# Optimization experiments

Hardware: AMD Instinct MI355X
Metric: run time of the kernel (lower is better)

The kernel has to match this reference:

```python
import jax, jax.numpy as jnp
import numpy as np

B, L, E = 4, 2048, 1024
H, HS = 16, 64  # head_num, head_size; E == H*HS


def setup_inputs() -> dict:
    key = jax.random.key(0)
    k1, k2, k3 = jax.random.split(key, 3)
    x = jax.random.normal(k1, (B, L, E), dtype=jnp.float32)
    W_attn = jax.random.normal(k2, (E, 3 * H * HS), dtype=jnp.float32) * (E ** -0.5)
    W_ffn = jax.random.normal(k3, (H * HS, E), dtype=jnp.float32) * ((H * HS) ** -0.5)
    return {"x": x, "W_attn": W_attn, "W_ffn": W_ffn}


def reference(x, W_attn, W_ffn):
    b, l, _ = x.shape
    z = x @ W_attn  # [B, L, 3*H*HS]
    # NOTE: original splits as (k, q, v) in that order
    k, q, v = jnp.split(z, 3, axis=2)
    k = k.reshape(b, l, H, HS).transpose(0, 2, 1, 3)  # [B,H,L,HS]
    q = q.reshape(b, l, H, HS).transpose(0, 2, 1, 3)
    v = v.reshape(b, l, H, HS).transpose(0, 2, 1, 3)
    # scores[i, j] = k_i . q_j (k plays the row role, q the column role)
    scores = jnp.einsum('bhid,bhjd->bhij', k, q) / (HS ** 0.5)
    idx = jnp.arange(l)
    causal = idx[None, :] > idx[:, None]  # True where j > i (masked out)
    scores = jnp.where(causal[None, None], -jnp.inf, scores)
    attn = jax.nn.softmax(scores, axis=-1)  # softmax over j (the q index)
    y = jnp.einsum('bhij,bhjd->bhid', attn, v)  # [B,H,L,HS]
    y = y.transpose(0, 2, 1, 3).reshape(b, l, H * HS)
    return y @ W_ffn
```

## Files before the change

### kernel.cpp

```cpp
#include <hip/hip_runtime.h>
#include <hip/hip_bf16.h>

typedef __attribute__((ext_vector_type(8))) short bf16x8;
typedef __attribute__((ext_vector_type(4))) float f32x4;

__device__ __forceinline__ short f2b(float f) {
    unsigned u = __builtin_bit_cast(unsigned, f);
    unsigned r = (u + 0x7FFFu + ((u >> 16) & 1u)) >> 16;
    return (short)r;
}

__device__ __forceinline__ unsigned cvt_pk_bf16(float lo, float hi) {
    unsigned r;
    asm("v_cvt_pk_bf16_f32 %0, %1, %2" : "=v"(r) : "v"(lo), "v"(hi));
    return r;
}

__device__ __forceinline__ void gload_lds16(const void* g, void* l) {
    __builtin_amdgcn_global_load_lds((const __attribute__((address_space(1))) unsigned*)g,
                                     (__attribute__((address_space(3))) unsigned*)l, 16, 0, 0);
}

__global__ void conv_swz(const float* __restrict__ in, short* __restrict__ out, long nch) {
    long i = (long)blockIdx.x * blockDim.x + threadIdx.x;
    long stride = (long)gridDim.x * blockDim.x;
    for (; i < nch; i += stride) {
        long m = i >> 7;
        int ch = (int)(i & 127);
        int p = (ch & ~7) | ((ch ^ (int)m) & 7);
        const float4* s = (const float4*)(in + i * 8);
        float4 a = s[0], b = s[1];
        bf16x8 ov;
        ov[0] = f2b(a.x); ov[1] = f2b(a.y); ov[2] = f2b(a.z); ov[3] = f2b(a.w);
        ov[4] = f2b(b.x); ov[5] = f2b(b.y); ov[6] = f2b(b.z); ov[7] = f2b(b.w);
        *(bf16x8*)(out + (m << 10) + p * 8) = ov;
    }
}

__global__ void transpose_swz(const float* __restrict__ in, short* __restrict__ outT, int R, int C) {
    __shared__ float t[32][33];
    int c0 = blockIdx.x * 32, r0 = blockIdx.y * 32;
    int tx = threadIdx.x, ty = threadIdx.y;
    #pragma unroll
    for (int j = 0; j < 4; ++j)
        t[ty + j * 8][tx] = in[(long)(r0 + ty + j * 8) * C + c0 + tx];
    __syncthreads();
    #pragma unroll
    for (int j = 0; j < 4; ++j) {
        int n = c0 + ty + j * 8;
        int k = r0 + tx;
        int kp = (k & ~63) | ((((k >> 3) ^ n) & 7) << 3) | (k & 7);
        outT[(long)n * R + kp] = f2b(t[tx][ty + j * 8]);
    }
}

template<int MODE>
__launch_bounds__(256, 2)
__global__ void gemm_nt(const short* __restrict__ A, const short* __restrict__ Bt,
                        int M, int N, int K,
                        short* __restrict__ qrole, short* __restrict__ krole,
                        short* __restrict__ vT, float* __restrict__ out) {
    __shared__ __align__(16) short As[128][64];
    __shared__ __align__(16) short Bs[128][64];
    const int tid = threadIdx.x;
    const int lane = tid & 63;
    const int wid = tid >> 6;
    const int wm = wid >> 1, wn = wid & 1;
    const int m0 = blockIdx.y * 128, n0 = blockIdx.x * 128;
    const int r16 = lane & 15, g = lane >> 4;
    const int sw = r16 & 7;
    const char* Ab = (const char*)A;
    const char* Bb = (const char*)Bt;
    const long Kb = (long)K * 2;
    f32x4 acc[4][4] = {};
    for (int k0 = 0; k0 < K; k0 += 64) {
        #pragma unroll
        for (int it = 0; it < 4; ++it) {
            int id = it * 256 + tid;
            int r = id >> 3, cch = id & 7;
            gload_lds16(Ab + (long)(m0 + r) * Kb + k0 * 2 + cch * 16, (char*)As + id * 16);
            gload_lds16(Bb + (long)(n0 + r) * Kb + k0 * 2 + cch * 16, (char*)Bs + id * 16);
        }
        __syncthreads();
        #pragma unroll
        for (int kk = 0; kk < 2; ++kk) {
            bf16x8 af[4], bfr[4];
            #pragma unroll
            for (int m = 0; m < 4; ++m)
                af[m] = *(const bf16x8*)&As[wm * 64 + m * 16 + r16][((kk * 4 + g) ^ sw) * 8];
            #pragma unroll
            for (int n = 0; n < 4; ++n)
                bfr[n] = *(const bf16x8*)&Bs[wn * 64 + n * 16 + r16][((kk * 4 + g) ^ sw) * 8];
            #pragma unroll
            for (int m = 0; m < 4; ++m)
                #pragma unroll
                for (int n = 0; n < 4; ++n)
                    acc[m][n] = __builtin_amdgcn_mfma_f32_16x16x32_bf16(af[m], bfr[n], acc[m][n], 0, 0, 0);
        }
        __syncthreads();
    }
    #pragma unroll
    for (int m = 0; m < 4; ++m) {
        #pragma unroll
        for (int n = 0; n < 4; ++n) {
            #pragma unroll
            for (int r = 0; r < 4; ++r) {
                int row = m0 + wm * 64 + m * 16 + g * 4 + r;
                int col = n0 + wn * 64 + n * 16 + r16;
                float v = acc[m][n][r];
                if (MODE == 0) {
                    int which = col >> 10, cc = col & 1023;
                    int h = cc >> 6, d = cc & 63;
                    int b = row >> 11, li = row & 2047;
                    int bh = b * 16 + h;
                    if (which == 0)      qrole[((long)bh * 2048 + li) * 64 + d] = f2b(v * 0.18033688f);
                    else if (which == 1) krole[((long)bh * 2048 + li) * 64 + (d ^ ((li & 7) << 3))] = f2b(v);
                    else                 vT[((long)bh * 64 + d) * 2048 + ((li & ~63) | ((li & 63) ^ ((d & 7) << 3)))] = f2b(v);
                } else {
                    out[(long)row * N + col] = v;
                }
            }
        }
    }
}

__launch_bounds__(256, 3)
__global__ void attn_kernel(const short* __restrict__ qrole, const short* __restrict__ krole,
                            const short* __restrict__ vT, short* __restrict__ y) {
    __shared__ __align__(16) short K_lds[2][64][64];
    __shared__ __align__(16) short V_lds[2][64][64];
    __shared__ __align__(16) short P_lds[4][16][72];
    const int tid = threadIdx.x, lane = tid & 63, w = tid >> 6;
    const int r16 = lane & 15, g = lane >> 4;
    const int idb = blockIdx.x;
    const int bh = idb & 63;
    const int c = 15 - (idb >> 6);
    const int q0 = c << 7;
    const int T = 2 * c + 2;
    const short* qb = qrole + (long)bh * (2048 * 64);
    const char* kbyte = (const char*)(krole + (long)bh * (2048 * 64));
    const char* vbyte = (const char*)(vT + (long)bh * (64 * 2048));
    const int b = bh >> 4, h = bh & 15;

    bf16x8 qf[2][2];
    #pragma unroll
    for (int m = 0; m < 2; ++m)
        #pragma unroll
        for (int ks = 0; ks < 2; ++ks)
            qf[m][ks] = *(const bf16x8*)&qb[(long)(q0 + m * 64 + w * 16 + r16) * 64 + ks * 32 + g * 8];

    f32x4 o[2][4] = {};
    float mr[2], lr[2];
    #pragma unroll
    for (int m = 0; m < 2; ++m) { mr[m] = -1e30f; lr[m] = 0.f; }

    {
        char* kdst = (char*)&K_lds[0][0][0];
        char* vdst = (char*)&V_lds[0][0][0];
        #pragma unroll
        for (int it = 0; it < 2; ++it) {
            int cid = it * 256 + tid;
            long r = cid >> 3; int cch = cid & 7;
            gload_lds16(kbyte + r * 128 + cch * 16, kdst + cid * 16);
            gload_lds16(vbyte + r * 4096 + cch * 16, vdst + cid * 16);
        }
    }

    for (int t = 0; t < T; ++t) {
        __syncthreads();
        const int cur = t & 1;
        if (t + 1 < T) {
            const long jn = (long)(t + 1) << 6;
            char* kdst = (char*)&K_lds[cur ^ 1][0][0];
            char* vdst = (char*)&V_lds[cur ^ 1][0][0];
            #pragma unroll
            for (int it = 0; it < 2; ++it) {
                int cid = it * 256 + tid;
                long r = cid >> 3; int cch = cid & 7;
                gload_lds16(kbyte + (jn + r) * 128 + cch * 16, kdst + cid * 16);
                gload_lds16(vbyte + r * 4096 + jn * 2 + cch * 16, vdst + cid * 16);
            }
        }
        const int jt = t << 6;
        const char* kbase = (const char*)&K_lds[cur][0][0];
        const char* vbase = (const char*)&V_lds[cur][0][0];
        const int swz = (r16 & 7) << 4;

        #pragma unroll
        for (int m = 0; m < 2; ++m) {
            const int qbase = q0 + m * 64 + w * 16;
            if (jt > qbase + 15) continue;

            f32x4 s[4] = {};
            #pragma unroll
            for (int ks = 0; ks < 2; ++ks)
                #pragma unroll
                for (int n = 0; n < 4; ++n) {
                    bf16x8 kf = *(const bf16x8*)(kbase + (n * 16 + r16) * 128 + ((ks * 64 + g * 16) ^ swz));
                    s[n] = __builtin_amdgcn_mfma_f32_16x16x32_bf16(kf, qf[m][ks], s[n], 0, 0, 0);
                }
            if (jt + 63 > qbase) {
                const int i = qbase + r16;
                #pragma unroll
                for (int n = 0; n < 4; ++n)
                    #pragma unroll
                    for (int r = 0; r < 4; ++r)
                        if (jt + n * 16 + g * 4 + r > i) s[n][r] = -1e30f;
            }
            float tm = s[0][0];
            #pragma unroll
            for (int n = 0; n < 4; ++n)
                #pragma unroll
                for (int r = 0; r < 4; ++r)
                    tm = fmaxf(tm, s[n][r]);
            tm = fmaxf(tm, __shfl_xor(tm, 16));
            tm = fmaxf(tm, __shfl_xor(tm, 32));
            if (__any(tm > mr[m] + 11.5f)) {
                float mn = fmaxf(mr[m], tm);
                float sc = exp2f(mr[m] - mn);
                mr[m] = mn;
                lr[m] *= sc;
                float scr[4];
                #pragma unroll
                for (int r = 0; r < 4; ++r) scr[r] = __shfl(sc, (g << 2) + r);
                #pragma unroll
                for (int nd = 0; nd < 4; ++nd)
                    #pragma unroll
                    for (int r = 0; r < 4; ++r)
                        o[m][nd][r] *= scr[r];
            }
            float lsum = 0.f;
            #pragma unroll
            for (int n = 0; n < 4; ++n) {
                float p0 = exp2f(s[n][0] - mr[m]);
                float p1 = exp2f(s[n][1] - mr[m]);
                float p2 = exp2f(s[n][2] - mr[m]);
                float p3 = exp2f(s[n][3] - mr[m]);
                lsum += (p0 + p1) + (p2 + p3);
                unsigned w0 = cvt_pk_bf16(p0, p1);
                unsigned w1 = cvt_pk_bf16(p2, p3);
                unsigned long long dw = ((unsigned long long)w1 << 32) | w0;
                *(unsigned long long*)&P_lds[w][r16][n * 16 + g * 4] = dw;
            }
            lsum += __shfl_xor(lsum, 16);
            lsum += __shfl_xor(lsum, 32);
            lr[m] += lsum;
            #pragma unroll
            for (int ks = 0; ks < 2; ++ks) {
                bf16x8 pf = *(const bf16x8*)&P_lds[w][r16][ks * 32 + g * 8];
                #pragma unroll
                for (int nd = 0; nd < 4; ++nd) {
                    bf16x8 vf = *(const bf16x8*)(vbase + (nd * 16 + r16) * 128 + ((ks * 64 + g * 16) ^ swz));
                    o[m][nd] = __builtin_amdgcn_mfma_f32_16x16x32_bf16(pf, vf, o[m][nd], 0, 0, 0);
                }
            }
        }
    }
    #pragma unroll
    for (int m = 0; m < 2; ++m) {
        float inv[4];
        #pragma unroll
        for (int r = 0; r < 4; ++r) inv[r] = 1.0f / __shfl(lr[m], (g << 2) + r);
        const int li0 = q0 + m * 64 + w * 16 + (g << 2);
        #pragma unroll
        for (int nd = 0; nd < 4; ++nd)
            #pragma unroll
            for (int r = 0; r < 4; ++r) {
                int li = li0 + r;
                int sub = ((nd * 2 + (r16 >> 3)) ^ li) & 7;
                int kp = h * 64 + sub * 8 + (r16 & 7);
                y[(long)(b * 2048 + li) * 1024 + kp] = f2b(o[m][nd][r] * inv[r]);
            }
    }
}

extern "C" void kernel_launch(void* const* d_in, const int* in_sizes, int n_in,
                              void* d_out, int out_size, void* d_ws, size_t ws_size,
                              hipStream_t stream) {
    const float* x  = (const float*)d_in[0];
    const float* Wa = (const float*)d_in[1];
    const float* Wf = (const float*)d_in[2];
    float* out = (float*)d_out;
    char* ws = (char*)d_ws;
    short* xb  = (short*)(ws);
    short* wab = (short*)(ws + (16l << 20));
    short* wfb = (short*)(ws + (22l << 20));
    short* qr  = (short*)(ws + (24l << 20));
    short* kr  = (short*)(ws + (40l << 20));
    short* vt  = (short*)(ws + (56l << 20));

    conv_swz<<<2048, 256, 0, stream>>>(x, xb, (long)8192 * 128);
    transpose_swz<<<dim3(96, 32), dim3(32, 8), 0, stream>>>(Wa, wab, 1024, 3072);
    transpose_swz<<<dim3(32, 32), dim3(32, 8), 0, stream>>>(Wf, wfb, 1024, 1024);
    gemm_nt<0><<<dim3(24, 64), 256, 0, stream>>>(xb, wab, 8192, 3072, 1024, qr, kr, vt, nullptr);
    attn_kernel<<<1024, 256, 0, stream>>>(qr, kr, vt, xb);
    gemm_nt<1><<<dim3(8, 64), 256, 0, stream>>>(xb, wfb, 8192, 1024, 1024, nullptr, nullptr, nullptr, out);
}
```

Baseline: 179.1 us.

## Tune attention kernel: raw exp, swizzled P tile, setprio, block reorder, occupancy

Several attention-kernel changes land together. exp2f is replaced with a raw v_exp_f32, and the padded P tile becomes an XOR-swizzled 64-wide layout to save LDS. MFMA sections are wrapped in s_setprio, global-to-LDS load addresses are precomputed outside the loop, and query-chunk blocks are remapped to interleave long and short causal workloads. Launch bounds rise to 4 waves-per-SIMD for both the GEMM and attention kernels, which tightens register budgets and risks spills.

```diff
diff --git a/kernel.cpp b/kernel.cpp
--- a/kernel.cpp
+++ b/kernel.cpp
@@ -13,6 +13,12 @@
 __device__ __forceinline__ unsigned cvt_pk_bf16(float lo, float hi) {
     unsigned r;
     asm("v_cvt_pk_bf16_f32 %0, %1, %2" : "=v"(r) : "v"(lo), "v"(hi));
+    return r;
+}
+
+__device__ __forceinline__ float fexp2(float x) {
+    float r;
+    asm("v_exp_f32 %0, %1" : "=v"(r) : "v"(x));
     return r;
 }
 
@@ -55,7 +61,7 @@
 }
 
 template<int MODE>
-__launch_bounds__(256, 2)
+__launch_bounds__(256, 4)
 __global__ void gemm_nt(const short* __restrict__ A, const short* __restrict__ Bt,
                         int M, int N, int K,
                         short* __restrict__ qrole, short* __restrict__ krole,
@@ -124,17 +130,19 @@
     }
 }
 
-__launch_bounds__(256, 3)
+__launch_bounds__(256, 4)
 __global__ void attn_kernel(const short* __restrict__ qrole, const short* __restrict__ krole,
                             const short* __restrict__ vT, short* __restrict__ y) {
     __shared__ __align__(16) short K_lds[2][64][64];
     __shared__ __align__(16) short V_lds[2][64][64];
-    __shared__ __align__(16) short P_lds[4][16][72];
+    __shared__ __align__(16) short P_lds[4][16][64];
     const int tid = threadIdx.x, lane = tid & 63, w = tid >> 6;
     const int r16 = lane & 15, g = lane >> 4;
     const int idb = blockIdx.x;
     const int bh = idb & 63;
-    const int c = 15 - (idb >> 6);
+    const int u = idb >> 8;
+    const int a = (idb >> 6) & 3;
+    const int c = (u == 0) ? (15 - a) : (u == 1) ? a : (u == 2) ? (11 - a) : (4 + a);
     const int q0 = c << 7;
     const int T = 2 * c + 2;
     const short* qb = qrole + (long)bh * (2048 * 64);
@@ -154,37 +162,39 @@
     #pragma unroll
     for (int m = 0; m < 2; ++m) { mr[m] = -1e30f; lr[m] = 0.f; }
 
-    {
-        char* kdst = (char*)&K_lds[0][0][0];
-        char* vdst = (char*)&V_lds[0][0][0];
-        #pragma unroll
-        for (int it = 0; it < 2; ++it) {
-            int cid = it * 256 + tid;
-            long r = cid >> 3; int cch = cid & 7;
-            gload_lds16(kbyte + r * 128 + cch * 16, kdst + cid * 16);
-            gload_lds16(vbyte + r * 4096 + cch * 16, vdst + cid * 16);
-        }
-    }
+    const int rr = tid >> 3, cch = tid & 7;
+    const char* kg0 = kbyte + rr * 128 + cch * 16;
+    const char* kg1 = kbyte + (32 + rr) * 128 + cch * 16;
+    const char* vg0 = vbyte + rr * 4096 + cch * 16;
+    const char* vg1 = vbyte + (32 + rr) * 4096 + cch * 16;
+    char* Kb_ = (char*)&K_lds[0][0][0];
+    char* Vb_ = (char*)&V_lds[0][0][0];
+    const int ld0 = tid * 16, ld1 = (256 + tid) * 16;
+
+    gload_lds16(kg0, Kb_ + ld0);
+    gload_lds16(kg1, Kb_ + ld1);
+    gload_lds16(vg0, Vb_ + ld0);
+    gload_lds16(vg1, Vb_ + ld1);
+
+    const int psw = (r16 & 7) << 4;
+    char* prow = (char*)&P_lds[w][r16][0];
 
     for (int t = 0; t < T; ++t) {
         __syncthreads();
         const int cur = t & 1;
         if (t + 1 < T) {
-            const long jn = (long)(t + 1) << 6;
-            char* kdst = (char*)&K_lds[cur ^ 1][0][0];
-            char* vdst = (char*)&V_lds[cur ^ 1][0][0];
-            #pragma unroll
-            for (int it = 0; it < 2; ++it) {
-                int cid = it * 256 + tid;
-                long r = cid >> 3; int cch = cid & 7;
-                gload_lds16(kbyte + (jn + r) * 128 + cch * 16, kdst + cid * 16);
-                gload_lds16(vbyte + r * 4096 + jn * 2 + cch * 16, vdst + cid * 16);
-            }
+            long adv = (long)(t + 1) * 8192;
+            long advv = (long)(t + 1) * 128;
+            char* kdst = Kb_ + (cur ^ 1) * 8192;
+            char* vdst = Vb_ + (cur ^ 1) * 8192;
+            gload_lds16(kg0 + adv, kdst + ld0);
+            gload_lds16(kg1 + adv, kdst + ld1);
+            gload_lds16(vg0 + advv, vdst + ld0);
+            gload_lds16(vg1 + advv, vdst + ld1);
         }
         const int jt = t << 6;
-        const char* kbase = (const char*)&K_lds[cur][0][0];
-        const char* vbase = (const char*)&V_lds[cur][0][0];
-        const int swz = (r16 & 7) << 4;
+        const char* kbase = Kb_ + cur * 8192;
+        const char* vbase = Vb_ + cur * 8192;
 
         #pragma unroll
         for (int m = 0; m < 2; ++m) {
@@ -192,13 +202,15 @@
             if (jt > qbase + 15) continue;
 
             f32x4 s[4] = {};
+            __builtin_amdgcn_s_setprio(1);
             #pragma unroll
             for (int ks = 0; ks < 2; ++ks)
                 #pragma unroll
                 for (int n = 0; n < 4; ++n) {
-                    bf16x8 kf = *(const bf16x8*)(kbase + (n * 16 + r16) * 128 + ((ks * 64 + g * 16) ^ swz));
+                    bf16x8 kf = *(const bf16x8*)(kbase + (n * 16 + r16) * 128 + ((ks * 64 + g * 16) ^ psw));
                     s[n] = __builtin_amdgcn_mfma_f32_16x16x32_bf16(kf, qf[m][ks], s[n], 0, 0, 0);
                 }
+            __builtin_amdgcn_s_setprio(0);
             if (jt + 63 > qbase) {
                 const int i = qbase + r16;
                 #pragma unroll
@@ -207,17 +219,16 @@
                     for (int r = 0; r < 4; ++r)
                         if (jt + n * 16 + g * 4 + r > i) s[n][r] = -1e30f;
             }
-            float tm = s[0][0];
-            #pragma unroll
-            for (int n = 0; n < 4; ++n)
-                #pragma unroll
-                for (int r = 0; r < 4; ++r)
-                    tm = fmaxf(tm, s[n][r]);
+            float t0 = fmaxf(fmaxf(s[0][0], s[0][1]), fmaxf(s[0][2], s[0][3]));
+            float t1 = fmaxf(fmaxf(s[1][0], s[1][1]), fmaxf(s[1][2], s[1][3]));
+            float t2 = fmaxf(fmaxf(s[2][0], s[2][1]), fmaxf(s[2][2], s[2][3]));
+            float t3 = fmaxf(fmaxf(s[3][0], s[3][1]), fmaxf(s[3][2], s[3][3]));
+            float tm = fmaxf(fmaxf(t0, t1), fmaxf(t2, t3));
             tm = fmaxf(tm, __shfl_xor(tm, 16));
             tm = fmaxf(tm, __shfl_xor(tm, 32));
             if (__any(tm > mr[m] + 11.5f)) {
                 float mn = fmaxf(mr[m], tm);
-                float sc = exp2f(mr[m] - mn);
+                float sc = fexp2(mr[m] - mn);
                 mr[m] = mn;
                 lr[m] *= sc;
                 float scr[4];
@@ -229,31 +240,37 @@
                     for (int r = 0; r < 4; ++r)
                         o[m][nd][r] *= scr[r];
             }
-            float lsum = 0.f;
+            float p[4][4];
             #pragma unroll
             for (int n = 0; n < 4; ++n) {
-                float p0 = exp2f(s[n][0] - mr[m]);
-                float p1 = exp2f(s[n][1] - mr[m]);
-                float p2 = exp2f(s[n][2] - mr[m]);
-                float p3 = exp2f(s[n][3] - mr[m]);
-                lsum += (p0 + p1) + (p2 + p3);
-                unsigned w0 = cvt_pk_bf16(p0, p1);
-                unsigned w1 = cvt_pk_bf16(p2, p3);
+                p[n][0] = fexp2(s[n][0] - mr[m]);
+                p[n][1] = fexp2(s[n][1] - mr[m]);
+                p[n][2] = fexp2(s[n][2] - mr[m]);
+                p[n][3] = fexp2(s[n][3] - mr[m]);
+                unsigned w0 = cvt_pk_bf16(p[n][0], p[n][1]);
+                unsigned w1 = cvt_pk_bf16(p[n][2], p[n][3]);
                 unsigned long long dw = ((unsigned long long)w1 << 32) | w0;
-                *(unsigned long long*)&P_lds[w][r16][n * 16 + g * 4] = dw;
-            }
+                *(unsigned long long*)(prow + ((n * 32 + g * 8) ^ psw)) = dw;
+            }
+            float l0 = (p[0][0] + p[0][1]) + (p[0][2] + p[0][3]);
+            float l1 = (p[1][0] + p[1][1]) + (p[1][2] + p[1][3]);
+            float l2 = (p[2][0] + p[2][1]) + (p[2][2] + p[2][3]);
+            float l3 = (p[3][0] + p[3][1]) + (p[3][2] + p[3][3]);
+            float lsum = (l0 + l1) + (l2 + l3);
             lsum += __shfl_xor(lsum, 16);
             lsum += __shfl_xor(lsum, 32);
             lr[m] += lsum;
+            __builtin_amdgcn_s_setprio(1);
             #pragma unroll
             for (int ks = 0; ks < 2; ++ks) {
-                bf16x8 pf = *(const bf16x8*)&P_lds[w][r16][ks * 32 + g * 8];
+                bf16x8 pf = *(const bf16x8*)(prow + ((ks * 64 + g * 16) ^ psw));
                 #pragma unroll
                 for (int nd = 0; nd < 4; ++nd) {
-                    bf16x8 vf = *(const bf16x8*)(vbase + (nd * 16 + r16) * 128 + ((ks * 64 + g * 16) ^ swz));
+                    bf16x8 vf = *(const bf16x8*)(vbase + (nd * 16 + r16) * 128 + ((ks * 64 + g * 16) ^ psw));
                     o[m][nd] = __builtin_amdgcn_mfma_f32_16x16x32_bf16(pf, vf, o[m][nd], 0, 0, 0);
                 }
             }
+            __builtin_amdgcn_s_setprio(0);
         }
     }
     #pragma unroll
```

New measurement: 174.5 us. 1.03x faster.
